# Kernel optimization log

Hardware: AMD Instinct MI355X
Metric: run time of the kernel (lower is better)

Reference implementation:

```python
import jax, jax.numpy as jnp
import numpy as np

N_PARTICLES = 512
N_DIM = 3
N_KERNELS = 32
N_TIME = 10
BATCH = 8
EPS = 1e-6


def rbf_kernels(d, mu, neg_log_gamma, derivative=False):
    # d: [..., 1], mu/neg_log_gamma: [K] -> normalized rbf kernels [..., K]
    inv_gamma2 = jnp.square(jnp.exp(neg_log_gamma))
    diff = d - mu
    rbfs = jnp.exp(-jnp.square(diff) * inv_gamma2)
    srbf = rbfs.sum(-1, keepdims=True)
    kernels = rbfs / (EPS + srbf)
    if not derivative:
        return kernels, None
    drbfs = -2.0 * diff * inv_gamma2 * rbfs
    sdrbf = drbfs.sum(-1, keepdims=True)
    dkernels = drbfs / (EPS + srbf) - rbfs * sdrbf / jnp.square(EPS + srbf)
    return kernels, dkernels


def setup_inputs() -> dict:
    key = jax.random.key(0)
    k_t, k_x, k_w = jax.random.split(key, 3)
    t = jax.random.uniform(k_t, (1,), dtype=jnp.float32)
    x = jax.random.normal(k_x, (BATCH, N_PARTICLES * N_DIM), dtype=jnp.float32)
    mus = jnp.linspace(0.0, 1.0, N_KERNELS, dtype=jnp.float32)
    neg_log_gammas = -jnp.log(jnp.full((N_KERNELS,), 0.3, dtype=jnp.float32))
    mus_time = jnp.linspace(0.0, 1.0, N_TIME, dtype=jnp.float32)
    neg_log_gammas_time = -jnp.log(jnp.full((N_TIME,), 0.3, dtype=jnp.float32))
    weights = jax.random.normal(k_w, (N_KERNELS, N_TIME), dtype=jnp.float32) * np.float32(np.sqrt(1.0 / N_KERNELS))
    bias = jnp.zeros((1, N_TIME), dtype=jnp.float32)
    importance = jnp.zeros((N_KERNELS,), dtype=jnp.float32)
    return dict(t=t, x=x, mus=mus, neg_log_gammas=neg_log_gammas,
                mus_time=mus_time, neg_log_gammas_time=neg_log_gammas_time,
                weights=weights, bias=bias, importance=importance)


def reference(t, x, mus, neg_log_gammas, mus_time, neg_log_gammas_time, weights, bias, importance):
    B = x.shape[0]
    xp = x.reshape(B, N_PARTICLES, N_DIM)
    # pairwise distance vectors r[b,i,j] = x_i - x_j : [B,N,N,D]
    r = xp[:, :, None, :] - xp[:, None, :, :]
    d = jnp.sqrt(jnp.square(r).sum(-1) + EPS)[..., None]          # [B,N,N,1]
    rbfs, d_rbfs = rbf_kernels(d, mus, neg_log_gammas, derivative=True)  # [B,N,N,K]
    force_mag = (rbfs + jnp.square(importance)) @ weights + bias  # [B,N,N,T]
    d_force_mag = d_rbfs @ weights                                # [B,N,N,T]
    trbfs, _ = rbf_kernels(t, mus_time, neg_log_gammas_time)      # [T]
    force_mag = (force_mag * trbfs).sum(-1, keepdims=True)        # [B,N,N,1]
    d_force_mag = (d_force_mag * trbfs).sum(-1, keepdims=True)
    # mask replicates bgflow's remove_diagonal in distance_vectors (self-pairs excluded)
    mask = (1.0 - jnp.eye(N_PARTICLES, dtype=x.dtype))[None, :, :, None]
    forces = (r * force_mag * mask).sum(-2).reshape(B, -1)        # [B, N*D]
    divergence = ((d * d_force_mag + N_DIM * force_mag) * mask).reshape(B, -1).sum(-1, keepdims=True)
    return forces, -divergence
```

## Files before the change

### kernel.cpp

```cpp
#include <hip/hip_runtime.h>

#define N_P   512
#define N_DIMC 3
#define N_K   32
#define N_T   10
#define BATCHC 8
#define EPSC  1e-6f
#define LOG2E 1.4426950408889634f

typedef float f2 __attribute__((ext_vector_type(2)));

__device__ __forceinline__ float rfl(float v) {
    return __int_as_float(__builtin_amdgcn_readfirstlane(__float_as_int(v)));
}


__global__ __launch_bounds__(512) void
pair_kernel(const float* __restrict__ x,
            const float* __restrict__ t,
            const float* __restrict__ mus,
            const float* __restrict__ nlg,
            const float* __restrict__ mus_time,
            const float* __restrict__ nlg_time,
            const float* __restrict__ weights,
            const float* __restrict__ bias,
            const float* __restrict__ importance,
            float* __restrict__ out) {
    const int b     = blockIdx.x >> 7;
    const int itile = blockIdx.x & 127;

    __shared__ float sx[N_P], sy[N_P], sz[N_P];
    __shared__ float cws[70];
    __shared__ float trbf_l[N_T];
    __shared__ float red[8][4];

    const int tid = threadIdx.x;

    const float* xb = x + b * (N_P * N_DIMC);
#pragma unroll
    for (int idx = tid; idx < N_P * N_DIMC; idx += 512) {
        float v = xb[idx];
        int p = idx / 3;
        int c = idx - 3 * p;
        if (c == 0) sx[p] = v;
        else if (c == 1) sy[p] = v;
        else sz[p] = v;
    }

    if (tid < N_K) {
        float t0 = t[0];
        float r[N_T];
        float s = 0.f;
        for (int tt = 0; tt < N_T; ++tt) {
            float g = __expf(nlg_time[tt]);
            float diff = t0 - mus_time[tt];
            r[tt] = __expf(-diff * diff * g * g);
            s += r[tt];
        }
        float inv = 1.f / (EPSC + s);
        float w = 0.f;
        for (int tt = 0; tt < N_T; ++tt) w = fmaf(weights[tid * N_T + tt], r[tt] * inv, w);
        int pos = (tid < 16) ? (2 * tid) : (2 * (tid - 16) + 1);
        cws[pos] = w;
        if (tid == 0) {
            for (int tt = 0; tt < N_T; ++tt) trbf_l[tt] = r[tt] * inv;
        }
    } else if (tid >= 64 && tid < 80) {
        int kk = tid - 64;
        float g0 = __expf(nlg[0]);
        float c  = g0 * g0;
        float D  = mus[1] - mus[0];
        float s_lo = 1.f, s_hi = 1.f;
        if (kk < 15) {
            s_lo = __builtin_amdgcn_exp2f(-LOG2E * c * D * (mus[kk] + mus[kk + 1]));
            s_hi = __builtin_amdgcn_exp2f(-LOG2E * c * D * (mus[kk + 16] + mus[kk + 17]));
        }
        cws[32 + 2 * kk] = s_lo;
        cws[33 + 2 * kk] = s_hi;
        if (kk == 0) {
            cws[64] = -c * LOG2E;
            cws[65] = 2.f * c * D * LOG2E;
            cws[66] = -2.f * c;
            cws[67] = mus[16];
            cws[68] = D;
        }
    }
    __syncthreads();

    f2 w2[16], s2[16];
#pragma unroll
    for (int k = 0; k < 16; ++k) {
        w2[k] = (f2){rfl(cws[2 * k]),      rfl(cws[2 * k + 1])};
        s2[k] = (f2){rfl(cws[32 + 2 * k]), rfl(cws[33 + 2 * k])};
    }
    const float mcl2 = rfl(cws[64]);
    const float ku   = rfl(cws[65]);
    const float n2c  = rfl(cws[66]);
    const float mu16 = rfl(cws[67]);
    const float dlt  = rfl(cws[68]);

    if (tid == 0) {
        float c0 = 0.f;
        for (int tt = 0; tt < N_T; ++tt) c0 = fmaf(bias[tt], trbf_l[tt], c0);
        for (int kk = 0; kk < N_K; ++kk) {
            float im = importance[kk];
            float w = (kk < 16) ? cws[2 * kk] : cws[2 * (kk - 16) + 1];
            c0 = fmaf(im * im, w, c0);
        }
        cws[69] = c0;
    }
    __syncthreads();
    const float cterm = rfl(cws[69]);

    const int wid   = tid >> 6;
    const int lane  = tid & 63;
    const int i     = itile * 4 + (wid & 3);
    const int jbase = (wid >> 2) * (N_P / 2);

    const float xi_x = sx[i], xi_y = sy[i], xi_z = sz[i];

    float fx = 0.f, fy = 0.f, fz = 0.f, dva = 0.f, dvb = 0.f;

    for (int jj = 0; jj < N_P / 2 / 64; ++jj) {
        int j = jbase + jj * 64 + lane;
        float dx = xi_x - sx[j];
        float dy = xi_y - sy[j];
        float dz = xi_z - sz[j];
        float dsq = fmaf(dx, dx, fmaf(dy, dy, dz * dz)) + EPSC;
        float d = __builtin_amdgcn_sqrtf(dsq);

        float dh  = d - mu16;
        float alo = __builtin_amdgcn_exp2f(mcl2 * dsq);
        float ahi = __builtin_amdgcn_exp2f(mcl2 * dh * dh);
        float u   = __builtin_amdgcn_exp2f(ku * d);

        f2 a2    = (f2){alo, ahi};
        f2 u2    = (f2){u, u};
        f2 diff2 = (f2){d, dh};
        f2 md2   = (f2){-dlt, -dlt};
        f2 rs = (f2){0.f, 0.f}, wes = rs, dse = rs, wdse = rs;
#pragma unroll
        for (int k = 0; k < 16; ++k) {
            f2 wek = w2[k] * a2;
            rs   += a2;
            wes  += wek;
            dse  += diff2 * a2;
            wdse += diff2 * wek;
            f2 us = u2 * s2[k];
            a2    = a2 * us;
            diff2 = diff2 + md2;
        }
        float rsum = rs.x + rs.y;
        float we   = wes.x + wes.y;
        float ds   = dse.x + dse.y;
        float wds  = wdse.x + wdse.y;

        float inv  = __builtin_amdgcn_rcpf(EPSC + rsum);
        float fmag = fmaf(we, inv, cterm);
        float uu   = fmaf(-we * inv, ds, wds);
        float dfm  = (n2c * inv) * uu;

        bool self = (j == i);
        fmag = self ? 0.f : fmag;
        dfm  = self ? 0.f : dfm;

        fx  = fmaf(dx, fmag, fx);
        fy  = fmaf(dy, fmag, fy);
        fz  = fmaf(dz, fmag, fz);
        dva = fmaf(d, dfm, dva);
        dvb += fmag;
    }
    float dv = fmaf(3.f, dvb, dva);

#pragma unroll
    for (int off = 32; off >= 1; off >>= 1) {
        fx += __shfl_down(fx, off, 64);
        fy += __shfl_down(fy, off, 64);
        fz += __shfl_down(fz, off, 64);
        dv += __shfl_down(dv, off, 64);
    }
    if (lane == 0) {
        red[wid][0] = fx; red[wid][1] = fy; red[wid][2] = fz; red[wid][3] = dv;
    }
    __syncthreads();
    if (tid < 4) {
        int tt = tid;
        int ii = itile * 4 + tt;
        float tfx = red[tt][0] + red[tt + 4][0];
        float tfy = red[tt][1] + red[tt + 4][1];
        float tfz = red[tt][2] + red[tt + 4][2];
        float tdv = red[tt][3] + red[tt + 4][3];
        float* outf = out + (b * N_P + ii) * 3;
        outf[0] = tfx;
        outf[1] = tfy;
        outf[2] = tfz;
        atomicAdd(out + BATCHC * N_P * N_DIMC + b, -tdv);
    }
}

extern "C" void kernel_launch(void* const* d_in, const int* in_sizes, int n_in,
                              void* d_out, int out_size, void* d_ws, size_t ws_size,
                              hipStream_t stream) {
    const float* t          = (const float*)d_in[0];
    const float* x          = (const float*)d_in[1];
    const float* mus        = (const float*)d_in[2];
    const float* nlg        = (const float*)d_in[3];
    const float* mus_time   = (const float*)d_in[4];
    const float* nlg_time   = (const float*)d_in[5];
    const float* weights    = (const float*)d_in[6];
    const float* bias       = (const float*)d_in[7];
    const float* importance = (const float*)d_in[8];
    float* out = (float*)d_out;

    pair_kernel<<<BATCHC * (N_P / 4), 512, 0, stream>>>(
        x, t, mus, nlg, mus_time, nlg_time, weights, bias, importance, out);
}
```

Measured before the change: 87.14 us.

## Rewrite RBF recurrence as geometric multiplier and assign one particle per wave

The inner 16-step loop now advances each Gaussian term with a multiplier that itself follows a geometric sequence (q^2 per step), so the per-term scale table and the per-step diff update are no longer needed. The derivative sums become weighted sums over mu, folded using precomputed w*mu products. Each wave now covers a whole row of 512 j values for its own particle, which halves the grid and removes the shared-memory cross-wave reduction and its extra barrier. The cost is another 32-entry register table and slightly different floating-point rounding, since mu-weighted sums are subtracted from d times the totals.

```diff
diff --git a/kernel.cpp b/kernel.cpp
--- a/kernel.cpp
+++ b/kernel.cpp
@@ -26,13 +26,12 @@
             const float* __restrict__ bias,
             const float* __restrict__ importance,
             float* __restrict__ out) {
-    const int b     = blockIdx.x >> 7;
-    const int itile = blockIdx.x & 127;
+    const int b     = blockIdx.x >> 6;
+    const int itile = blockIdx.x & 63;
 
     __shared__ float sx[N_P], sy[N_P], sz[N_P];
-    __shared__ float cws[70];
+    __shared__ float cws[104];
     __shared__ float trbf_l[N_T];
-    __shared__ float red[8][4];
 
     const int tid = threadIdx.x;
 
@@ -67,39 +66,28 @@
         }
     } else if (tid >= 64 && tid < 80) {
         int kk = tid - 64;
-        float g0 = __expf(nlg[0]);
-        float c  = g0 * g0;
-        float D  = mus[1] - mus[0];
-        float s_lo = 1.f, s_hi = 1.f;
-        if (kk < 15) {
-            s_lo = __builtin_amdgcn_exp2f(-LOG2E * c * D * (mus[kk] + mus[kk + 1]));
-            s_hi = __builtin_amdgcn_exp2f(-LOG2E * c * D * (mus[kk + 16] + mus[kk + 17]));
-        }
-        cws[32 + 2 * kk] = s_lo;
-        cws[33 + 2 * kk] = s_hi;
+        cws[32 + 2 * kk] = mus[kk];
+        cws[33 + 2 * kk] = mus[kk + 16];
         if (kk == 0) {
-            cws[64] = -c * LOG2E;
-            cws[65] = 2.f * c * D * LOG2E;
-            cws[66] = -2.f * c;
-            cws[67] = mus[16];
-            cws[68] = D;
+            float g0 = __expf(nlg[0]);
+            float c  = g0 * g0;
+            float D  = mus[1] - mus[0];
+            float cdd = c * D * D;
+            cws[96]  = -c * LOG2E;
+            cws[97]  = 2.f * c * D * LOG2E;
+            cws[98]  = -2.f * c;
+            cws[99]  = mus[16];
+            cws[100] = __expf(-cdd);
+            cws[101] = __expf(-33.f * cdd);
+            cws[102] = __expf(-2.f * cdd);
         }
     }
     __syncthreads();
 
-    f2 w2[16], s2[16];
-#pragma unroll
-    for (int k = 0; k < 16; ++k) {
-        w2[k] = (f2){rfl(cws[2 * k]),      rfl(cws[2 * k + 1])};
-        s2[k] = (f2){rfl(cws[32 + 2 * k]), rfl(cws[33 + 2 * k])};
-    }
-    const float mcl2 = rfl(cws[64]);
-    const float ku   = rfl(cws[65]);
-    const float n2c  = rfl(cws[66]);
-    const float mu16 = rfl(cws[67]);
-    const float dlt  = rfl(cws[68]);
-
-    if (tid == 0) {
+    if (tid < 16) {
+        cws[64 + 2 * tid] = cws[32 + 2 * tid] * cws[2 * tid];
+        cws[65 + 2 * tid] = cws[33 + 2 * tid] * cws[2 * tid + 1];
+    } else if (tid == 16) {
         float c0 = 0.f;
         for (int tt = 0; tt < N_T; ++tt) c0 = fmaf(bias[tt], trbf_l[tt], c0);
         for (int kk = 0; kk < N_K; ++kk) {
@@ -107,22 +95,37 @@
             float w = (kk < 16) ? cws[2 * kk] : cws[2 * (kk - 16) + 1];
             c0 = fmaf(im * im, w, c0);
         }
-        cws[69] = c0;
+        cws[103] = c0;
     }
     __syncthreads();
-    const float cterm = rfl(cws[69]);
-
-    const int wid   = tid >> 6;
-    const int lane  = tid & 63;
-    const int i     = itile * 4 + (wid & 3);
-    const int jbase = (wid >> 2) * (N_P / 2);
+
+    f2 w2[16], mu2[16], wm2[16];
+#pragma unroll
+    for (int k = 0; k < 16; ++k) {
+        w2[k]  = (f2){rfl(cws[2 * k]),      rfl(cws[2 * k + 1])};
+        mu2[k] = (f2){rfl(cws[32 + 2 * k]), rfl(cws[33 + 2 * k])};
+        wm2[k] = (f2){rfl(cws[64 + 2 * k]), rfl(cws[65 + 2 * k])};
+    }
+    const float mcl2  = rfl(cws[96]);
+    const float ku    = rfl(cws[97]);
+    const float n2c   = rfl(cws[98]);
+    const float mu16  = rfl(cws[99]);
+    const float q     = rfl(cws[100]);
+    const float q33   = rfl(cws[101]);
+    const float qqs   = rfl(cws[102]);
+    const float cterm = rfl(cws[103]);
+    const f2 qq2 = (f2){qqs, qqs};
+
+    const int wid  = tid >> 6;
+    const int lane = tid & 63;
+    const int i    = (itile << 3) + wid;
 
     const float xi_x = sx[i], xi_y = sy[i], xi_z = sz[i];
 
     float fx = 0.f, fy = 0.f, fz = 0.f, dva = 0.f, dvb = 0.f;
 
-    for (int jj = 0; jj < N_P / 2 / 64; ++jj) {
-        int j = jbase + jj * 64 + lane;
+    for (int jj = 0; jj < N_P / 64; ++jj) {
+        int j = (jj << 6) + lane;
         float dx = xi_x - sx[j];
         float dy = xi_y - sy[j];
         float dz = xi_z - sz[j];
@@ -134,28 +137,31 @@
         float ahi = __builtin_amdgcn_exp2f(mcl2 * dh * dh);
         float u   = __builtin_amdgcn_exp2f(ku * d);
 
-        f2 a2    = (f2){alo, ahi};
-        f2 u2    = (f2){u, u};
-        f2 diff2 = (f2){d, dh};
-        f2 md2   = (f2){-dlt, -dlt};
-        f2 rs = (f2){0.f, 0.f}, wes = rs, dse = rs, wdse = rs;
-#pragma unroll
-        for (int k = 0; k < 16; ++k) {
-            f2 wek = w2[k] * a2;
-            rs   += a2;
-            wes  += wek;
-            dse  += diff2 * a2;
-            wdse += diff2 * wek;
-            f2 us = u2 * s2[k];
-            a2    = a2 * us;
-            diff2 = diff2 + md2;
-        }
-        float rsum = rs.x + rs.y;
-        float we   = wes.x + wes.y;
-        float ds   = dse.x + dse.y;
-        float wds  = wdse.x + wdse.y;
+        f2 a2 = (f2){alo, ahi};
+        f2 m2 = (f2){u * q, u * q33};
+        f2 rs = (f2){0.f, 0.f}, wes = rs, ms = rs, wms = rs;
+#pragma unroll
+        for (int k = 0; k < 15; ++k) {
+            rs  += a2;
+            wes += w2[k]  * a2;
+            ms  += mu2[k] * a2;
+            wms += wm2[k] * a2;
+            a2   = a2 * m2;
+            m2   = m2 * qq2;
+        }
+        rs  += a2;
+        wes += w2[15]  * a2;
+        ms  += mu2[15] * a2;
+        wms += wm2[15] * a2;
+
+        float rsum  = rs.x + rs.y;
+        float we    = wes.x + wes.y;
+        float msum  = ms.x + ms.y;
+        float wmsum = wms.x + wms.y;
 
         float inv  = __builtin_amdgcn_rcpf(EPSC + rsum);
+        float ds   = fmaf(d, rsum, -msum);
+        float wds  = fmaf(d, we,   -wmsum);
         float fmag = fmaf(we, inv, cterm);
         float uu   = fmaf(-we * inv, ds, wds);
         float dfm  = (n2c * inv) * uu;
@@ -180,21 +186,11 @@
         dv += __shfl_down(dv, off, 64);
     }
     if (lane == 0) {
-        red[wid][0] = fx; red[wid][1] = fy; red[wid][2] = fz; red[wid][3] = dv;
-    }
-    __syncthreads();
-    if (tid < 4) {
-        int tt = tid;
-        int ii = itile * 4 + tt;
-        float tfx = red[tt][0] + red[tt + 4][0];
-        float tfy = red[tt][1] + red[tt + 4][1];
-        float tfz = red[tt][2] + red[tt + 4][2];
-        float tdv = red[tt][3] + red[tt + 4][3];
-        float* outf = out + (b * N_P + ii) * 3;
-        outf[0] = tfx;
-        outf[1] = tfy;
-        outf[2] = tfz;
-        atomicAdd(out + BATCHC * N_P * N_DIMC + b, -tdv);
+        float* outf = out + (b * N_P + i) * 3;
+        outf[0] = fx;
+        outf[1] = fy;
+        outf[2] = fz;
+        atomicAdd(out + BATCHC * N_P * N_DIMC + b, -dv);
     }
 }
 
@@ -212,6 +208,6 @@
     const float* importance = (const float*)d_in[8];
     float* out = (float*)d_out;
 
-    pair_kernel<<<BATCHC * (N_P / 4), 512, 0, stream>>>(
+    pair_kernel<<<BATCHC * (N_P / 8), 512, 0, stream>>>(
         x, t, mus, nlg, mus_time, nlg_time, weights, bias, importance, out);
 }
```

Result: slower. 125.8 us (+44.3%).
